# Kernel tuning notes

Hardware: AMD Instinct MI355X
Metric: run time of the kernel (lower is better)

The kernel has to match this reference:

```python
import jax, jax.numpy as jnp
import numpy as np

NCONF = 500      # configurations in batch
APC = 40         # atoms per configuration
NATOMS = NCONF * APC
ND = 64          # descriptor length
H = 128          # hidden width
NPAIRS = NATOMS * 20   # neighbor pairs
NDERIV = 3 * NPAIRS    # one row per (pair, cartesian axis)


def _mlp(x, W1, b1, W2, b2, W3, b3):
    h = jax.nn.sigmoid(x @ W1 + b1)
    h = jax.nn.sigmoid(h @ W2 + b2)
    return h @ W3 + b3  # [natoms, 1] per-atom energies


def setup_inputs() -> dict:
    key = jax.random.key(0)
    ks = jax.random.split(key, 8)
    x = jax.random.normal(ks[0], (NATOMS, ND), jnp.float32)
    xd = jax.random.normal(ks[1], (NDERIV, ND), jnp.float32)
    # contiguous config ids per atom
    indices = jnp.repeat(jnp.arange(NCONF, dtype=jnp.int32), APC)
    atoms_per_structure = jnp.full((NCONF,), APC, jnp.int32)
    types = jnp.zeros((NATOMS,), jnp.int32)
    # per-pair atom/neighbor ids, repeated for x/y/z rows
    pair_i = jax.random.randint(ks[2], (NPAIRS,), 0, NATOMS, jnp.int32)
    pair_j = jax.random.randint(ks[3], (NPAIRS,), 0, NATOMS, jnp.int32)
    unique_i = jnp.repeat(pair_i, 3)
    unique_j = jnp.repeat(pair_j, 3)
    axis = jnp.tile(jnp.arange(3, dtype=jnp.int32), NPAIRS)
    xd_indx = jnp.stack([jnp.repeat(pair_i, 3), jnp.repeat(pair_j, 3), axis], axis=1)
    # MLP parameters (fan-in scaled)
    W1 = jax.random.normal(ks[4], (ND, H), jnp.float32) / np.sqrt(ND)
    W2 = jax.random.normal(ks[5], (H, H), jnp.float32) / np.sqrt(H)
    W3 = jax.random.normal(ks[6], (H, 1), jnp.float32) / np.sqrt(H)
    b1 = jnp.zeros((H,), jnp.float32)
    b2 = jnp.zeros((H,), jnp.float32)
    b3 = jnp.zeros((1,), jnp.float32)
    return {"x": x, "xd": xd, "indices": indices,
            "atoms_per_structure": atoms_per_structure, "types": types,
            "xd_indx": xd_indx, "unique_i": unique_i, "unique_j": unique_j,
            "W1": W1, "b1": b1, "W2": W2, "b2": b2, "W3": W3, "b3": b3,
            "natoms": NATOMS}


def reference(x, xd, indices, atoms_per_structure, types, xd_indx,
              unique_i, unique_j, W1, b1, W2, b2, W3, b3, natoms):
    nconf = atoms_per_structure.shape[0]
    per_atom_energies = _mlp(x, W1, b1, W2, b2, W3, b3)[:, 0]  # [natoms]
    # energy: contract per-atom energies into per-config totals
    predicted_energy_total = jax.ops.segment_sum(per_atom_energies, indices,
                                                 num_segments=nconf)
    # dE/dD: gradient of total energy w.r.t. descriptors (vjp with ones)
    dEdD = jax.grad(lambda xx: jnp.sum(_mlp(xx, W1, b1, W2, b2, W3, b3)))(x)
    # gather dE/dD at neighbor rows, multiply by dD/dR, reduce over descriptor dim
    per_row = jnp.einsum('nd,nd->n', xd, dEdD[unique_i])  # [NDERIV]
    # scatter-add into (atom j, axis); equivalent to torch's three index_add_
    # followed by sum over descriptor dim and interleaved (fx,fy,fz) flatten
    axis = xd_indx[:, 2]
    flat_idx = unique_j * 3 + axis
    predicted_forces = jax.ops.segment_sum(per_row, flat_idx,
                                           num_segments=3 * natoms)
    return (predicted_energy_total, predicted_forces)
```

## Files before the change

kernel.cpp:

```cpp
#include <hip/hip_runtime.h>

typedef float f32x4 __attribute__((ext_vector_type(4)));
typedef __bf16 bf16x8 __attribute__((ext_vector_type(8)));
typedef unsigned int u32x4 __attribute__((ext_vector_type(4)));

#define TT 32

#define PW1_HI   0
#define PW1_LO   8192
#define PW2_HI   16384
#define PW2_LO   32768
#define PW2T_HI  49152
#define PW2T_LO  65536
#define PW1T_HI  81920
#define PW1T_LO  90112
#define PW_SLOTS 49152

__global__ void zero_kernel(float* __restrict__ p, int n) {
    int i = blockIdx.x * blockDim.x + threadIdx.x;
    if (i < n) p[i] = 0.f;
}

__device__ __forceinline__ void bf16split(float x, unsigned short& hi, unsigned short& lo) {
    unsigned u = __float_as_uint(x);
    unsigned r = (u + 0x7FFFu + ((u >> 16) & 1u)) >> 16;
    hi = (unsigned short)r;
    float hf = __uint_as_float(r << 16);
    unsigned u2 = __float_as_uint(x - hf);
    unsigned r2 = (u2 + 0x7FFFu + ((u2 >> 16) & 1u)) >> 16;
    lo = (unsigned short)r2;
}

__device__ __forceinline__ void split2(float a, float b, unsigned& hw, unsigned& lw) {
    unsigned ua = __float_as_uint(a);
    unsigned ra = (ua + 0x7FFFu + ((ua >> 16) & 1u)) >> 16;
    unsigned ua2 = __float_as_uint(a - __uint_as_float(ra << 16));
    unsigned la = (ua2 + 0x7FFFu + ((ua2 >> 16) & 1u)) >> 16;
    unsigned ub = __float_as_uint(b);
    unsigned rb = (ub + 0x7FFFu + ((ub >> 16) & 1u)) >> 16;
    unsigned ub2 = __float_as_uint(b - __uint_as_float(rb << 16));
    unsigned lb = (ub2 + 0x7FFFu + ((ub2 >> 16) & 1u)) >> 16;
    hw = ra | (rb << 16);
    lw = la | (lb << 16);
}

__global__ void pack_weights(const float* __restrict__ W1, const float* __restrict__ W2,
                             unsigned short* __restrict__ pw) {
    int s = blockIdx.x * blockDim.x + threadIdx.x;
    if (s >= PW_SLOTS) return;
    int slot, NS, hiOff, loOff; const float* src; bool tr;
    if (s < 8192)       { slot = s;         NS = 8; hiOff = PW1_HI;  loOff = PW1_LO;  tr = false; src = W1; }
    else if (s < 24576) { slot = s - 8192;  NS = 8; hiOff = PW2_HI;  loOff = PW2_LO;  tr = false; src = W2; }
    else if (s < 40960) { slot = s - 24576; NS = 8; hiOff = PW2T_HI; loOff = PW2T_LO; tr = true;  src = W2; }
    else                { slot = s - 40960; NS = 4; hiOff = PW1T_HI; loOff = PW1T_LO; tr = true;  src = W1; }
    int j = slot & 7, lane = (slot >> 3) & 63, rest = slot >> 9;
    int ns = rest % NS, ks = rest / NS;
    int k = ks * 32 + ((lane >> 4) & 3) * 8 + j;
    int n = ns * 16 + (lane & 15);
    float v = tr ? src[n * 128 + k] : src[k * 128 + n];
    unsigned short hi, lo;
    bf16split(v, hi, lo);
    pw[hiOff + slot] = hi;
    pw[loOff + slot] = lo;
}

__global__ __launch_bounds__(256, 2) void mlp_mfma(
    const float* __restrict__ x,
    const float* __restrict__ b1, const float* __restrict__ b2,
    const float* __restrict__ W3, const float* __restrict__ b3,
    const int* __restrict__ indices,
    const unsigned short* __restrict__ pw,
    float* __restrict__ energy, float* __restrict__ dEdD, int natoms)
{
    __shared__ float xs[TT * 64];
    __shared__ float h1s[TT * 128];
    __shared__ float g2s[TT * 128];

    const int tid = threadIdx.x;
    const int l   = tid & 63;
    const int w   = tid >> 6;
    const int col = l & 15;
    const int rg  = l >> 4;
    const int msub = w >> 1;
    const int half = w & 1;
    const int a0 = blockIdx.x * TT;
    const int mrow = msub * 16 + col;

    #pragma unroll
    for (int p = 0; p < 2; ++p) {
        int idx = tid + p * 256;
        int r = idx >> 4, c = idx & 15;
        int a = a0 + r;
        f32x4 v = {0.f, 0.f, 0.f, 0.f};
        if (a < natoms) v = *(const f32x4*)(x + (size_t)a * 64 + c * 4);
        *(f32x4*)(xs + r * 64 + ((c ^ (r & 7)) << 2)) = v;
    }
    __syncthreads();

    auto loadA = [&](const float* buf, int stride, int kbase, bf16x8& ah, bf16x8& al) {
        int key = mrow & 7;
        int c0 = kbase >> 2;
        f32x4 f0 = *(const f32x4*)(buf + mrow * stride + (((c0    ) ^ key) << 2));
        f32x4 f1 = *(const f32x4*)(buf + mrow * stride + (((c0 + 1) ^ key) << 2));
        u32x4 H, L;
        unsigned hw, lw;
        split2(f0[0], f0[1], hw, lw); H[0] = hw; L[0] = lw;
        split2(f0[2], f0[3], hw, lw); H[1] = hw; L[1] = lw;
        split2(f1[0], f1[1], hw, lw); H[2] = hw; L[2] = lw;
        split2(f1[2], f1[3], hw, lw); H[3] = hw; L[3] = lw;
        ah = __builtin_bit_cast(bf16x8, H);
        al = __builtin_bit_cast(bf16x8, L);
    };
    auto loadB = [&](int hiOff, int loOff, int NS, int ks, int nsub, bf16x8& bh, bf16x8& bl) {
        size_t idx = ((size_t)(ks * NS + nsub) * 64 + l) * 8;
        bh = __builtin_bit_cast(bf16x8, *(const u32x4*)(pw + hiOff + idx));
        bl = __builtin_bit_cast(bf16x8, *(const u32x4*)(pw + loOff + idx));
    };

    bf16x8 ah0, al0, ah1, al1, ah2, al2, ah3, al3;

    #define KSTEP(HIOFF, LOOFF, NS, KS, NSUB, AH, AL)                              \
        {                                                                          \
            bf16x8 bh, bl;                                                         \
            loadB(HIOFF, LOOFF, NS, KS, NSUB, bh, bl);                             \
            acc = __builtin_amdgcn_mfma_f32_16x16x32_bf16(AH, bh, acc, 0, 0, 0);   \
            acc = __builtin_amdgcn_mfma_f32_16x16x32_bf16(AL, bh, acc, 0, 0, 0);   \
            acc = __builtin_amdgcn_mfma_f32_16x16x32_bf16(AH, bl, acc, 0, 0, 0);   \
        }

    loadA(xs, 64,  0 + rg * 8, ah0, al0);
    loadA(xs, 64, 32 + rg * 8, ah1, al1);
    #pragma unroll
    for (int ns = 0; ns < 4; ++ns) {
        int nsub = half * 4 + ns, n0 = nsub * 16;
        float bv = b1[n0 + col];
        f32x4 acc = {bv, bv, bv, bv};
        KSTEP(PW1_HI, PW1_LO, 8, 0, nsub, ah0, al0)
        KSTEP(PW1_HI, PW1_LO, 8, 1, nsub, ah1, al1)
        #pragma unroll
        for (int r2 = 0; r2 < 4; ++r2) {
            int m = msub * 16 + rg * 4 + r2, k = n0 + col;
            float h = 1.f / (1.f + expf(-acc[r2]));
            h1s[m * 128 + ((((k >> 2)) ^ (m & 7)) << 2) + (k & 3)] = h;
        }
    }
    __syncthreads();

    loadA(h1s, 128,  0 + rg * 8, ah0, al0);
    loadA(h1s, 128, 32 + rg * 8, ah1, al1);
    loadA(h1s, 128, 64 + rg * 8, ah2, al2);
    loadA(h1s, 128, 96 + rg * 8, ah3, al3);
    float e0 = 0.f, e1 = 0.f, e2 = 0.f, e3 = 0.f;
    #pragma unroll
    for (int ns = 0; ns < 4; ++ns) {
        int nsub = half * 4 + ns, n0 = nsub * 16;
        float bv = b2[n0 + col];
        f32x4 acc = {bv, bv, bv, bv};
        KSTEP(PW2_HI, PW2_LO, 8, 0, nsub, ah0, al0)
        KSTEP(PW2_HI, PW2_LO, 8, 1, nsub, ah1, al1)
        KSTEP(PW2_HI, PW2_LO, 8, 2, nsub, ah2, al2)
        KSTEP(PW2_HI, PW2_LO, 8, 3, nsub, ah3, al3)
        float w3v = W3[n0 + col];
        #pragma unroll
        for (int r2 = 0; r2 < 4; ++r2) {
            float h2 = 1.f / (1.f + expf(-acc[r2]));
            float ec = h2 * w3v;
            if (r2 == 0) e0 += ec; else if (r2 == 1) e1 += ec;
            else if (r2 == 2) e2 += ec; else e3 += ec;
            float g = w3v * h2 * (1.f - h2);
            int m = msub * 16 + rg * 4 + r2, k = n0 + col;
            g2s[m * 128 + ((((k >> 2)) ^ (m & 7)) << 2) + (k & 3)] = g;
        }
    }
    {
        e0 += __shfl_xor(e0, 1); e0 += __shfl_xor(e0, 2); e0 += __shfl_xor(e0, 4); e0 += __shfl_xor(e0, 8);
        e1 += __shfl_xor(e1, 1); e1 += __shfl_xor(e1, 2); e1 += __shfl_xor(e1, 4); e1 += __shfl_xor(e1, 8);
        e2 += __shfl_xor(e2, 1); e2 += __shfl_xor(e2, 2); e2 += __shfl_xor(e2, 4); e2 += __shfl_xor(e2, 8);
        e3 += __shfl_xor(e3, 1); e3 += __shfl_xor(e3, 2); e3 += __shfl_xor(e3, 4); e3 += __shfl_xor(e3, 8);
        if (col == 0) {
            float b3v = (half == 0) ? b3[0] : 0.f;
            int ab = a0 + msub * 16 + rg * 4;
            if (ab + 0 < natoms) atomicAdd(&energy[indices[ab + 0]], e0 + b3v);
            if (ab + 1 < natoms) atomicAdd(&energy[indices[ab + 1]], e1 + b3v);
            if (ab + 2 < natoms) atomicAdd(&energy[indices[ab + 2]], e2 + b3v);
            if (ab + 3 < natoms) atomicAdd(&energy[indices[ab + 3]], e3 + b3v);
        }
    }
    __syncthreads();

    loadA(g2s, 128,  0 + rg * 8, ah0, al0);
    loadA(g2s, 128, 32 + rg * 8, ah1, al1);
    loadA(g2s, 128, 64 + rg * 8, ah2, al2);
    loadA(g2s, 128, 96 + rg * 8, ah3, al3);
    #pragma unroll
    for (int ns = 0; ns < 4; ++ns) {
        int nsub = half * 4 + ns, n0 = nsub * 16;
        f32x4 acc = {0.f, 0.f, 0.f, 0.f};
        KSTEP(PW2T_HI, PW2T_LO, 8, 0, nsub, ah0, al0)
        KSTEP(PW2T_HI, PW2T_LO, 8, 1, nsub, ah1, al1)
        KSTEP(PW2T_HI, PW2T_LO, 8, 2, nsub, ah2, al2)
        KSTEP(PW2T_HI, PW2T_LO, 8, 3, nsub, ah3, al3)
        #pragma unroll
        for (int r2 = 0; r2 < 4; ++r2) {
            int m = msub * 16 + rg * 4 + r2, k = n0 + col;
            int off = m * 128 + ((((k >> 2)) ^ (m & 7)) << 2) + (k & 3);
            float hv = h1s[off];
            h1s[off] = acc[r2] * hv * (1.f - hv);
        }
    }
    __syncthreads();

    loadA(h1s, 128,  0 + rg * 8, ah0, al0);
    loadA(h1s, 128, 32 + rg * 8, ah1, al1);
    loadA(h1s, 128, 64 + rg * 8, ah2, al2);
    loadA(h1s, 128, 96 + rg * 8, ah3, al3);
    #pragma unroll
    for (int ns = 0; ns < 2; ++ns) {
        int nsub = half * 2 + ns, n0 = nsub * 16;
        f32x4 acc = {0.f, 0.f, 0.f, 0.f};
        KSTEP(PW1T_HI, PW1T_LO, 4, 0, nsub, ah0, al0)
        KSTEP(PW1T_HI, PW1T_LO, 4, 1, nsub, ah1, al1)
        KSTEP(PW1T_HI, PW1T_LO, 4, 2, nsub, ah2, al2)
        KSTEP(PW1T_HI, PW1T_LO, 4, 3, nsub, ah3, al3)
        #pragma unroll
        for (int r2 = 0; r2 < 4; ++r2) {
            int a = a0 + msub * 16 + rg * 4 + r2;
            if (a < natoms) dEdD[(size_t)a * 64 + n0 + col] = acc[r2];
        }
    }
    #undef KSTEP
}

__global__ __launch_bounds__(256) void force_kernel(
    const float* __restrict__ xd,
    const int* __restrict__ unique_i, const int* __restrict__ unique_j,
    const float* __restrict__ dEdD,
    float* __restrict__ forces, int nderiv)
{
    const int tid = threadIdx.x;
    const int lane = tid & 63;
    const int wib = tid >> 6;
    const int gwave = blockIdx.x * 4 + wib;
    const int nwaves = gridDim.x * 4;
    const int sub = lane >> 4;
    const int t = lane & 15;
    const int ngroups = (nderiv + 3) >> 2;

    for (int g = gwave; g < ngroups; g += nwaves) {
        const int r = g * 4 + sub;
        float p = 0.f;
        int jdst = 0, ax = 0;
        const bool valid = (r < nderiv);
        if (valid) {
            const int ai = unique_i[r];
            const float4 v = ((const float4*)(xd   + (size_t)r  * 64))[t];
            const float4 wv = ((const float4*)(dEdD + (size_t)ai * 64))[t];
            p = v.x * wv.x + v.y * wv.y + v.z * wv.z + v.w * wv.w;
            jdst = unique_j[r];
            ax = r % 3;
        }
        p += __shfl_xor(p, 1);
        p += __shfl_xor(p, 2);
        p += __shfl_xor(p, 4);
        p += __shfl_xor(p, 8);
        if (t == 0 && valid) atomicAdd(&forces[jdst * 3 + ax], p);
    }
}

extern "C" void kernel_launch(void* const* d_in, const int* in_sizes, int n_in,
                              void* d_out, int out_size, void* d_ws, size_t ws_size,
                              hipStream_t stream) {
    const float* x        = (const float*)d_in[0];
    const float* xd       = (const float*)d_in[1];
    const int*   indices  = (const int*)d_in[2];
    const int*   unique_i = (const int*)d_in[6];
    const int*   unique_j = (const int*)d_in[7];
    const float* W1       = (const float*)d_in[8];
    const float* b1       = (const float*)d_in[9];
    const float* W2       = (const float*)d_in[10];
    const float* b2       = (const float*)d_in[11];
    const float* W3       = (const float*)d_in[12];
    const float* b3       = (const float*)d_in[13];

    const int natoms = in_sizes[2];
    const int nconf  = in_sizes[3];
    const int nderiv = in_sizes[6];

    float* out    = (float*)d_out;
    float* energy = out;
    float* forces = out + nconf;
    float* dEdD   = (float*)d_ws;
    unsigned short* pw = (unsigned short*)((char*)d_ws + (size_t)natoms * 64 * 4);

    const int ntiles = (natoms + TT - 1) / TT;

    zero_kernel<<<(out_size + 255) / 256, 256, 0, stream>>>(out, out_size);
    pack_weights<<<(PW_SLOTS + 255) / 256, 256, 0, stream>>>(W1, W2, pw);
    mlp_mfma<<<ntiles, 256, 0, stream>>>(x, b1, b2, W3, b3, indices, pw,
                                         energy, dEdD, natoms);
    force_kernel<<<2048, 256, 0, stream>>>(xd, unique_i, unique_j, dEdD,
                                           forces, nderiv);
}
```

Before: 139.4 us.

## Merge zeroing into weight packing and unroll force loop by two groups

```diff
diff --git a/kernel.cpp b/kernel.cpp
--- a/kernel.cpp
+++ b/kernel.cpp
@@ -15,11 +15,6 @@
 #define PW1T_HI  81920
 #define PW1T_LO  90112
 #define PW_SLOTS 49152
-
-__global__ void zero_kernel(float* __restrict__ p, int n) {
-    int i = blockIdx.x * blockDim.x + threadIdx.x;
-    if (i < n) p[i] = 0.f;
-}
 
 __device__ __forceinline__ void bf16split(float x, unsigned short& hi, unsigned short& lo) {
     unsigned u = __float_as_uint(x);
@@ -44,9 +39,11 @@
     lw = la | (lb << 16);
 }
 
-__global__ void pack_weights(const float* __restrict__ W1, const float* __restrict__ W2,
-                             unsigned short* __restrict__ pw) {
+__global__ void zero_pack(const float* __restrict__ W1, const float* __restrict__ W2,
+                          unsigned short* __restrict__ pw,
+                          float* __restrict__ out, int out_size) {
     int s = blockIdx.x * blockDim.x + threadIdx.x;
+    if (s < out_size) out[s] = 0.f;
     if (s >= PW_SLOTS) return;
     int slot, NS, hiOff, loOff; const float* src; bool tr;
     if (s < 8192)       { slot = s;         NS = 8; hiOff = PW1_HI;  loOff = PW1_LO;  tr = false; src = W1; }
@@ -246,24 +243,41 @@
     const int t = lane & 15;
     const int ngroups = (nderiv + 3) >> 2;
 
-    for (int g = gwave; g < ngroups; g += nwaves) {
-        const int r = g * 4 + sub;
-        float p = 0.f;
-        int jdst = 0, ax = 0;
-        const bool valid = (r < nderiv);
-        if (valid) {
-            const int ai = unique_i[r];
-            const float4 v = ((const float4*)(xd   + (size_t)r  * 64))[t];
-            const float4 wv = ((const float4*)(dEdD + (size_t)ai * 64))[t];
-            p = v.x * wv.x + v.y * wv.y + v.z * wv.z + v.w * wv.w;
-            jdst = unique_j[r];
-            ax = r % 3;
-        }
-        p += __shfl_xor(p, 1);
-        p += __shfl_xor(p, 2);
-        p += __shfl_xor(p, 4);
-        p += __shfl_xor(p, 8);
-        if (t == 0 && valid) atomicAdd(&forces[jdst * 3 + ax], p);
+    for (int g = gwave; g < ngroups; g += 2 * nwaves) {
+        const int gB = g + nwaves;
+        float p0 = 0.f, p1 = 0.f;
+        int j0 = 0, x0 = 0, j1 = 0, x1 = 0;
+        bool v0 = false, v1 = false;
+        {
+            const int r = g * 4 + sub;
+            v0 = (r < nderiv);
+            if (v0) {
+                const int ai = unique_i[r];
+                const float4 v = ((const float4*)(xd   + (size_t)r  * 64))[t];
+                const float4 wv = ((const float4*)(dEdD + (size_t)ai * 64))[t];
+                p0 = v.x * wv.x + v.y * wv.y + v.z * wv.z + v.w * wv.w;
+                j0 = unique_j[r];
+                x0 = r % 3;
+            }
+        }
+        if (gB < ngroups) {
+            const int r = gB * 4 + sub;
+            v1 = (r < nderiv);
+            if (v1) {
+                const int ai = unique_i[r];
+                const float4 v = ((const float4*)(xd   + (size_t)r  * 64))[t];
+                const float4 wv = ((const float4*)(dEdD + (size_t)ai * 64))[t];
+                p1 = v.x * wv.x + v.y * wv.y + v.z * wv.z + v.w * wv.w;
+                j1 = unique_j[r];
+                x1 = r % 3;
+            }
+        }
+        p0 += __shfl_xor(p0, 1); p1 += __shfl_xor(p1, 1);
+        p0 += __shfl_xor(p0, 2); p1 += __shfl_xor(p1, 2);
+        p0 += __shfl_xor(p0, 4); p1 += __shfl_xor(p1, 4);
+        p0 += __shfl_xor(p0, 8); p1 += __shfl_xor(p1, 8);
+        if (t == 0 && v0) atomicAdd(&forces[j0 * 3 + x0], p0);
+        if (t == 0 && v1) atomicAdd(&forces[j1 * 3 + x1], p1);
     }
 }
 
@@ -293,9 +307,9 @@
     unsigned short* pw = (unsigned short*)((char*)d_ws + (size_t)natoms * 64 * 4);
 
     const int ntiles = (natoms + TT - 1) / TT;
-
-    zero_kernel<<<(out_size + 255) / 256, 256, 0, stream>>>(out, out_size);
-    pack_weights<<<(PW_SLOTS + 255) / 256, 256, 0, stream>>>(W1, W2, pw);
+    const int zp_n = (out_size > PW_SLOTS) ? out_size : PW_SLOTS;
+
+    zero_pack<<<(zp_n + 255) / 256, 256, 0, stream>>>(W1, W2, pw, out, out_size);
     mlp_mfma<<<ntiles, 256, 0, stream>>>(x, b1, b2, W3, b3, indices, pw,
                                          energy, dEdD, natoms);
     force_kernel<<<2048, 256, 0, stream>>>(xd, unique_i, unique_j, dEdD,
```

Result: faster. 133.2 us (median of 2 runs) (-4.4%).
